# Kernel tuning notes

Hardware: AMD Instinct MI355X
Metric: run time of the kernel (lower is better)

Reference implementation:

```python
import jax, jax.numpy as jnp
import numpy as np

N = 4096
IN_F = 128
OUT_F = 128
H = 4
D = OUT_F // H  # head_out = 32
SLOPE = 0.2
LN_EPS = 1e-5


def setup_inputs() -> dict:
    key = jax.random.key(0)
    k_x, k_adj, k_W, k_a = jax.random.split(key, 4)
    x = jax.random.normal(k_x, (N, IN_F), dtype=jnp.float32)
    adjacency = jax.random.randint(k_adj, (N, N), 0, 2).astype(jnp.bool_)
    # xavier-uniform-ish init scales
    w_std = float(np.sqrt(2.0 / (IN_F + H * D)))
    a_std = float(np.sqrt(2.0 / (H + 2 * D)))
    W = jax.random.normal(k_W, (H * D, IN_F), dtype=jnp.float32) * w_std  # torch Linear weight layout
    a = jax.random.normal(k_a, (H, 2 * D), dtype=jnp.float32) * a_std
    ln_gamma = jnp.ones((OUT_F,), dtype=jnp.float32)
    ln_beta = jnp.zeros((OUT_F,), dtype=jnp.float32)
    return {"x": x, "adjacency": adjacency, "W": W, "a": a,
            "ln_gamma": ln_gamma, "ln_beta": ln_beta}


def reference(x, adjacency, W, a, ln_gamma, ln_beta):
    # Wx: (N, H, D)
    Wx = (x @ W.T).reshape(N, H, D)
    # e[i,j,h] = leaky_relu( <Wx[i,h], a[h,:D]> + <Wx[j,h], a[h,D:]> )
    # (exact factorization of the original cat([Wx_i, Wx_j]) * a sum)
    alpha_i = jnp.einsum('nhd,hd->nh', Wx, a[:, :D])  # source/i term
    alpha_j = jnp.einsum('nhd,hd->nh', Wx, a[:, D:])  # neighbor/j term
    e = alpha_i[:, None, :] + alpha_j[None, :, :]      # (N, N, H)
    e = jnp.where(e >= 0, e, SLOPE * e)                # LeakyReLU
    e = jnp.where(adjacency[:, :, None], e, -jnp.inf)  # mask non-edges
    attn = jax.nn.softmax(e, axis=1)                   # softmax over j
    out = jnp.einsum('ijh,jhd->ihd', attn, Wx).reshape(N, H * D)
    y = out + x                                        # residual (dims match)
    mu = jnp.mean(y, axis=-1, keepdims=True)
    var = jnp.mean((y - mu) ** 2, axis=-1, keepdims=True)
    return ln_gamma * (y - mu) / jnp.sqrt(var + LN_EPS) + ln_beta
```

## Files before the change

kernel.cpp:

```cpp
#include <hip/hip_runtime.h>
#include <hip/hip_bf16.h>
#include <stdint.h>

#define NN 4096
#define SLOPE 0.2f
#define LOG2E 1.44269504088896340736f

typedef float f32x4 __attribute__((ext_vector_type(4)));
typedef float f32x2 __attribute__((ext_vector_type(2)));
typedef short s16x8 __attribute__((ext_vector_type(8)));
typedef unsigned u32x4 __attribute__((ext_vector_type(4)));

static __device__ __forceinline__ unsigned f32_to_bf16_rne(float f) {
    unsigned u = __builtin_bit_cast(unsigned, f);
    return (u + 0x7FFFu + ((u >> 16) & 1u)) >> 16;
}

__global__ __launch_bounds__(256) void k0_pack(const unsigned* __restrict__ src,
                                               unsigned* __restrict__ bits) {
    __shared__ int s_i32;
    const int t = threadIdx.x;
    if (t == 0) {
        int all_small = 1;
        for (int i = 0; i < 32; ++i) all_small &= (src[i] <= 1u);
        s_i32 = all_small;
    }
    __syncthreads();
    const long o = (long)blockIdx.x * 256 + t;
    unsigned m = 0;
    if (s_i32) {
        const u32x4* p = (const u32x4*)src + o * 8;
        #pragma unroll
        for (int g = 0; g < 8; ++g) {
            u32x4 v = p[g];
            m |= (v.x & 1u) << (g * 4) | (v.y & 1u) << (g * 4 + 1) |
                 (v.z & 1u) << (g * 4 + 2) | (v.w & 1u) << (g * 4 + 3);
        }
    } else {
        const u32x4* p = (const u32x4*)src + o * 2;
        #pragma unroll
        for (int g = 0; g < 2; ++g) {
            u32x4 v = p[g];
            unsigned d[4] = {v.x, v.y, v.z, v.w};
            #pragma unroll
            for (int q = 0; q < 4; ++q)
                #pragma unroll
                for (int b = 0; b < 4; ++b)
                    m |= ((d[q] >> (8 * b)) & 1u) << (g * 16 + q * 4 + b);
        }
    }
    bits[o] = m;
}

__global__ __launch_bounds__(256) void k1_wx(const float* __restrict__ x,
                                             const float* __restrict__ W,
                                             const float* __restrict__ a,
                                             unsigned short* __restrict__ wxb,
                                             float* __restrict__ ai_s,
                                             float* __restrict__ ajT_s) {
    __shared__ unsigned short WL[128 * 136];
    __shared__ unsigned short XL[16 * 136];
    __shared__ float WxF[16 * 132];

    const int t = threadIdx.x;
    const int i0 = blockIdx.x * 16;

    for (int p4 = t; p4 < 4096; p4 += 256) {
        f32x4 w4 = *(const f32x4*)(W + 4 * p4);
        unsigned lo = f32_to_bf16_rne(w4.x) | (f32_to_bf16_rne(w4.y) << 16);
        unsigned hi = f32_to_bf16_rne(w4.z) | (f32_to_bf16_rne(w4.w) << 16);
        int c = (4 * p4) >> 7, k = (4 * p4) & 127;
        *(unsigned long long*)&WL[c * 136 + k] =
            (unsigned long long)lo | ((unsigned long long)hi << 32);
    }
    for (int p4 = t; p4 < 512; p4 += 256) {
        f32x4 x4 = *(const f32x4*)(x + (long)i0 * 128 + 4 * p4);
        unsigned lo = f32_to_bf16_rne(x4.x) | (f32_to_bf16_rne(x4.y) << 16);
        unsigned hi = f32_to_bf16_rne(x4.z) | (f32_to_bf16_rne(x4.w) << 16);
        int r = (4 * p4) >> 7, k = (4 * p4) & 127;
        *(unsigned long long*)&XL[r * 136 + k] =
            (unsigned long long)lo | ((unsigned long long)hi << 32);
    }
    __syncthreads();

    const int w = t >> 6, l = t & 63, m = l & 15, q = l >> 4;
    f32x4 acc0 = {0.f, 0.f, 0.f, 0.f}, acc1 = {0.f, 0.f, 0.f, 0.f};
    #pragma unroll
    for (int ks = 0; ks < 4; ++ks) {
        s16x8 af = *(const s16x8*)&XL[m * 136 + ks * 32 + q * 8];
        s16x8 b0 = *(const s16x8*)&WL[(w * 32 + m) * 136 + ks * 32 + q * 8];
        s16x8 b1 = *(const s16x8*)&WL[(w * 32 + 16 + m) * 136 + ks * 32 + q * 8];
        acc0 = __builtin_amdgcn_mfma_f32_16x16x32_bf16(af, b0, acc0, 0, 0, 0);
        acc1 = __builtin_amdgcn_mfma_f32_16x16x32_bf16(af, b1, acc1, 0, 0, 0);
    }
    #pragma unroll
    for (int j2 = 0; j2 < 2; ++j2) {
        const int fblk = 2 * w + j2;
        f32x4 acc = j2 ? acc1 : acc0;
        #pragma unroll
        for (int reg = 0; reg < 4; ++reg) {
            float v = acc[reg];
            int row_g = i0 + q * 4 + reg;
            int kl = row_g & 31, jblk = row_g >> 5;
            wxb[(((jblk * 8 + fblk) * 64 + (kl >> 3) * 16 + m) << 3) + (kl & 7)] =
                (unsigned short)f32_to_bf16_rne(v);
            WxF[(q * 4 + reg) * 132 + fblk * 16 + m] = v;
        }
    }
    __syncthreads();
    if (t < 64) {
        int r = t >> 2, h = t & 3;
        float s_i = 0.f, s_j = 0.f;
        const float* ar = a + h * 64;
        #pragma unroll
        for (int d = 0; d < 32; ++d) {
            float wv = WxF[r * 132 + h * 32 + d];
            s_i += wv * ar[d];
            s_j += wv * ar[32 + d];
        }
        ai_s[(i0 + r) * 4 + h] = s_i * LOG2E;
        ajT_s[h * NN + i0 + r] = s_j * LOG2E;
    }
}

__global__ __launch_bounds__(1024, 4) void k2_attn(
        const float* __restrict__ x,
        const unsigned* __restrict__ adjbits,
        const unsigned short* __restrict__ wxb,
        const float* __restrict__ ai_s,
        const float* __restrict__ ajT_s,
        const float* __restrict__ gamma,
        const float* __restrict__ beta,
        float* __restrict__ out) {
    __shared__ float ajL[4][4096];
    __shared__ unsigned maskL[16][132];
    __shared__ float C_lds[4][16][32];
    __shared__ float l_lds[4][16];

    const int t = threadIdx.x;
    const int i0 = blockIdx.x * 16;
    const int w = t >> 6, l = t & 63;
    const int h = w & 3, p = w >> 2;
    const int m = l & 15, q = l >> 4;

    {
        const f32x4* src = (const f32x4*)ajT_s;
        f32x4* dst = (f32x4*)&ajL[0][0];
        #pragma unroll
        for (int g = 0; g < 4; ++g) dst[t + 1024 * g] = src[t + 1024 * g];
    }
    {
        #pragma unroll
        for (int g = 0; g < 2; ++g) {
            int idx = t + 1024 * g;
            int r = idx >> 7, c = idx & 127;
            maskL[r][c] = adjbits[(long)(i0 + r) * 128 + c];
        }
    }
    const float ai = ai_s[(i0 + m) * 4 + h];
    __syncthreads();

    const unsigned short* bp = wxb + ((2 * h) * 64 + l) * 8;
    const float* ajh = &ajL[h][0] + q * 8;

    f32x4 acc0 = {0.f, 0.f, 0.f, 0.f}, acc1 = {0.f, 0.f, 0.f, 0.f};
    float lpart = 0.f;

    for (int ks = p; ks < 128; ks += 4) {
        unsigned mq = (maskL[m][ks] >> (q * 8)) & 0xffu;
        f32x4 aj0 = *(const f32x4*)(ajh + ks * 32);
        f32x4 aj1 = *(const f32x4*)(ajh + ks * 32 + 4);
        s16x8 b0 = *(const s16x8*)(bp + ks * 4096);
        s16x8 b1 = *(const s16x8*)(bp + ks * 4096 + 512);

        float ev[8];
        #pragma unroll
        for (int e = 0; e < 8; ++e) {
            float s = ai + (e < 4 ? aj0[e] : aj1[e - 4]);
            s = fmaxf(s, SLOPE * s);
            float ex = __builtin_amdgcn_exp2f(s);
            ex = ((mq >> e) & 1u) ? ex : 0.0f;
            lpart += ex;
            ev[e] = ex;
        }
        union { s16x8 v; unsigned u[4]; } af;
        #pragma unroll
        for (int pr = 0; pr < 4; ++pr) {
            unsigned e0 = __builtin_bit_cast(unsigned, ev[2 * pr]);
            unsigned e1 = __builtin_bit_cast(unsigned, ev[2 * pr + 1]);
            af.u[pr] = __builtin_amdgcn_perm(e1, e0, 0x07060302);
        }
        acc0 = __builtin_amdgcn_mfma_f32_16x16x32_bf16(af.v, b0, acc0, 0, 0, 0);
        acc1 = __builtin_amdgcn_mfma_f32_16x16x32_bf16(af.v, b1, acc1, 0, 0, 0);
    }

    lpart += __shfl_xor(lpart, 16, 64);
    lpart += __shfl_xor(lpart, 32, 64);

    if (p == 0) {
        #pragma unroll
        for (int reg = 0; reg < 4; ++reg) {
            C_lds[h][q * 4 + reg][m] = acc0[reg];
            C_lds[h][q * 4 + reg][16 + m] = acc1[reg];
        }
        if (l < 16) l_lds[h][l] = lpart;
    }
    __syncthreads();
    if (p == 1) {
        #pragma unroll
        for (int reg = 0; reg < 4; ++reg) {
            C_lds[h][q * 4 + reg][m] += acc0[reg];
            C_lds[h][q * 4 + reg][16 + m] += acc1[reg];
        }
        if (l < 16) l_lds[h][l] += lpart;
    }
    __syncthreads();
    if (p == 2) {
        #pragma unroll
        for (int reg = 0; reg < 4; ++reg) {
            C_lds[h][q * 4 + reg][m] += acc0[reg];
            C_lds[h][q * 4 + reg][16 + m] += acc1[reg];
        }
        if (l < 16) l_lds[h][l] += lpart;
    }
    __syncthreads();
    if (p == 3) {
        #pragma unroll
        for (int reg = 0; reg < 4; ++reg) {
            C_lds[h][q * 4 + reg][m] += acc0[reg];
            C_lds[h][q * 4 + reg][16 + m] += acc1[reg];
        }
        if (l < 16) l_lds[h][l] += lpart;
    }
    __syncthreads();

    if (t < 512) {
        const int r = t >> 5, c32 = t & 31;
        const int f0 = c32 * 4;
        const int hh = f0 >> 5, cl = f0 & 31;
        const float linv = 1.0f / l_lds[hh][r];
        f32x4 xv = *(const f32x4*)(x + (long)(i0 + r) * 128 + f0);
        float y[4], s1 = 0.f, s2 = 0.f;
        #pragma unroll
        for (int kk = 0; kk < 4; ++kk) {
            float yy = C_lds[hh][r][cl + kk] * linv + xv[kk];
            y[kk] = yy; s1 += yy; s2 += yy * yy;
        }
        #pragma unroll
        for (int s = 1; s <= 16; s <<= 1) {
            s1 += __shfl_xor(s1, s, 64);
            s2 += __shfl_xor(s2, s, 64);
        }
        const float mean = s1 * (1.0f / 128.0f);
        const float var = s2 * (1.0f / 128.0f) - mean * mean;
        const float rstd = rsqrtf(var + 1e-5f);
        f32x4 gv = *(const f32x4*)(gamma + f0);
        f32x4 bv = *(const f32x4*)(beta + f0);
        f32x4 ov;
        #pragma unroll
        for (int kk = 0; kk < 4; ++kk)
            ov[kk] = gv[kk] * ((y[kk] - mean) * rstd) + bv[kk];
        *(f32x4*)(out + (long)(i0 + r) * 128 + f0) = ov;
    }
}

extern "C" void kernel_launch(void* const* d_in, const int* in_sizes, int n_in,
                              void* d_out, int out_size, void* d_ws, size_t ws_size,
                              hipStream_t stream) {
    const float* x = (const float*)d_in[0];
    const unsigned* adj_raw = (const unsigned*)d_in[1];
    const float* W = (const float*)d_in[2];
    const float* a = (const float*)d_in[3];
    const float* gamma = (const float*)d_in[4];
    const float* beta = (const float*)d_in[5];

    unsigned short* wxb = (unsigned short*)d_ws;
    float* ai_s = (float*)((char*)d_ws + (1 << 20));
    float* ajT_s = (float*)((char*)d_ws + (1 << 20) + (64 << 10));
    unsigned* adjbits = (unsigned*)((char*)d_ws + (2 << 20));

    k0_pack<<<2048, 256, 0, stream>>>(adj_raw, adjbits);
    k1_wx<<<256, 256, 0, stream>>>(x, W, a, wxb, ai_s, ajT_s);
    k2_attn<<<256, 1024, 0, stream>>>(x, adjbits, wxb, ai_s, ajT_s, gamma, beta,
                                      (float*)d_out);
}
```

Before: 136.4 us.

## Use fp8/bf8 MFMA for attention aggregation and merge pack and projection kernels

Stores the projected features as fp8 and the attention weights as bf8, so the aggregation runs on the 16x16x32 bf8/fp8 MFMA instead of bf16. The softmax denominator now comes from an extra MFMA against a constant all-ones fp8 vector instead of a scalar sum with shuffles. B-operand loads are prefetched one iteration ahead, and the adjacency-pack and projection kernels are merged into a single launch. This halves the feature bytes and launch count, but costs precision (3-bit mantissa on exp weights, 8-bit fp8 features), which risks tolerance failures.

```diff
diff --git a/kernel.cpp b/kernel.cpp
--- a/kernel.cpp
+++ b/kernel.cpp
@@ -7,7 +7,6 @@
 #define LOG2E 1.44269504088896340736f
 
 typedef float f32x4 __attribute__((ext_vector_type(4)));
-typedef float f32x2 __attribute__((ext_vector_type(2)));
 typedef short s16x8 __attribute__((ext_vector_type(8)));
 typedef unsigned u32x4 __attribute__((ext_vector_type(4)));
 
@@ -16,54 +15,56 @@
     return (u + 0x7FFFu + ((u >> 16) & 1u)) >> 16;
 }
 
-__global__ __launch_bounds__(256) void k0_pack(const unsigned* __restrict__ src,
-                                               unsigned* __restrict__ bits) {
-    __shared__ int s_i32;
+__global__ __launch_bounds__(256) void k01(const unsigned* __restrict__ adj_raw,
+                                           const float* __restrict__ x,
+                                           const float* __restrict__ W,
+                                           const float* __restrict__ a,
+                                           unsigned* __restrict__ bits,
+                                           unsigned* __restrict__ wxb8,
+                                           float* __restrict__ ai_s,
+                                           float* __restrict__ ajT_s) {
     const int t = threadIdx.x;
-    if (t == 0) {
-        int all_small = 1;
-        for (int i = 0; i < 32; ++i) all_small &= (src[i] <= 1u);
-        s_i32 = all_small;
-    }
-    __syncthreads();
-    const long o = (long)blockIdx.x * 256 + t;
-    unsigned m = 0;
-    if (s_i32) {
-        const u32x4* p = (const u32x4*)src + o * 8;
-        #pragma unroll
-        for (int g = 0; g < 8; ++g) {
-            u32x4 v = p[g];
-            m |= (v.x & 1u) << (g * 4) | (v.y & 1u) << (g * 4 + 1) |
-                 (v.z & 1u) << (g * 4 + 2) | (v.w & 1u) << (g * 4 + 3);
-        }
-    } else {
-        const u32x4* p = (const u32x4*)src + o * 2;
-        #pragma unroll
-        for (int g = 0; g < 2; ++g) {
-            u32x4 v = p[g];
-            unsigned d[4] = {v.x, v.y, v.z, v.w};
+    if (blockIdx.x < 2048) {
+        __shared__ int s_i32;
+        if (t == 0) {
+            int all_small = 1;
+            for (int i = 0; i < 32; ++i) all_small &= (adj_raw[i] <= 1u);
+            s_i32 = all_small;
+        }
+        __syncthreads();
+        const long o = (long)blockIdx.x * 256 + t;
+        unsigned mm = 0;
+        if (s_i32) {
+            const u32x4* p = (const u32x4*)adj_raw + o * 8;
             #pragma unroll
-            for (int q = 0; q < 4; ++q)
+            for (int g = 0; g < 8; ++g) {
+                u32x4 v = p[g];
+                mm |= (v.x & 1u) << (g * 4) | (v.y & 1u) << (g * 4 + 1) |
+                      (v.z & 1u) << (g * 4 + 2) | (v.w & 1u) << (g * 4 + 3);
+            }
+        } else {
+            const u32x4* p = (const u32x4*)adj_raw + o * 2;
+            #pragma unroll
+            for (int g = 0; g < 2; ++g) {
+                u32x4 v = p[g];
+                unsigned d[4] = {v.x, v.y, v.z, v.w};
                 #pragma unroll
-                for (int b = 0; b < 4; ++b)
-                    m |= ((d[q] >> (8 * b)) & 1u) << (g * 16 + q * 4 + b);
-        }
-    }
-    bits[o] = m;
-}
-
-__global__ __launch_bounds__(256) void k1_wx(const float* __restrict__ x,
-                                             const float* __restrict__ W,
-                                             const float* __restrict__ a,
-                                             unsigned short* __restrict__ wxb,
-                                             float* __restrict__ ai_s,
-                                             float* __restrict__ ajT_s) {
+                for (int qq = 0; qq < 4; ++qq)
+                    #pragma unroll
+                    for (int b = 0; b < 4; ++b)
+                        mm |= ((d[qq] >> (8 * b)) & 1u) << (g * 16 + qq * 4 + b);
+            }
+        }
+        bits[o] = mm;
+        return;
+    }
+
     __shared__ unsigned short WL[128 * 136];
     __shared__ unsigned short XL[16 * 136];
     __shared__ float WxF[16 * 132];
 
-    const int t = threadIdx.x;
-    const int i0 = blockIdx.x * 16;
+    const int bid = blockIdx.x - 2048;
+    const int i0 = bid * 16;
 
     for (int p4 = t; p4 < 4096; p4 += 256) {
         f32x4 w4 = *(const f32x4*)(W + 4 * p4);
@@ -93,19 +94,18 @@
         acc0 = __builtin_amdgcn_mfma_f32_16x16x32_bf16(af, b0, acc0, 0, 0, 0);
         acc1 = __builtin_amdgcn_mfma_f32_16x16x32_bf16(af, b1, acc1, 0, 0, 0);
     }
+    const int jblk = i0 >> 5;
+    const int qp = ((i0 & 16) + q * 4) >> 3;
+    const int ehalf = q & 1;
     #pragma unroll
     for (int j2 = 0; j2 < 2; ++j2) {
-        const int fblk = 2 * w + j2;
         f32x4 acc = j2 ? acc1 : acc0;
-        #pragma unroll
-        for (int reg = 0; reg < 4; ++reg) {
-            float v = acc[reg];
-            int row_g = i0 + q * 4 + reg;
-            int kl = row_g & 31, jblk = row_g >> 5;
-            wxb[(((jblk * 8 + fblk) * 64 + (kl >> 3) * 16 + m) << 3) + (kl & 7)] =
-                (unsigned short)f32_to_bf16_rne(v);
-            WxF[(q * 4 + reg) * 132 + fblk * 16 + m] = v;
-        }
+        unsigned u = (unsigned)__builtin_amdgcn_cvt_pk_fp8_f32(acc[0], acc[1], 0, false);
+        u = (unsigned)__builtin_amdgcn_cvt_pk_fp8_f32(acc[2], acc[3], (int)u, true);
+        wxb8[(((jblk * 4 + w) * 64 + qp * 16 + m) << 2) + j2 * 2 + ehalf] = u;
+        #pragma unroll
+        for (int reg = 0; reg < 4; ++reg)
+            WxF[(q * 4 + reg) * 132 + (2 * w + j2) * 16 + m] = acc[reg];
     }
     __syncthreads();
     if (t < 64) {
@@ -126,7 +126,7 @@
 __global__ __launch_bounds__(1024, 4) void k2_attn(
         const float* __restrict__ x,
         const unsigned* __restrict__ adjbits,
-        const unsigned short* __restrict__ wxb,
+        const unsigned* __restrict__ wxb8,
         const float* __restrict__ ai_s,
         const float* __restrict__ ajT_s,
         const float* __restrict__ gamma,
@@ -160,18 +160,21 @@
     const float ai = ai_s[(i0 + m) * 4 + h];
     __syncthreads();
 
-    const unsigned short* bp = wxb + ((2 * h) * 64 + l) * 8;
+    const unsigned* bp8 = wxb8 + ((h * 64 + l) << 2);
     const float* ajh = &ajL[h][0] + q * 8;
+    const long ONESB = 0x3838383838383838L;
 
     f32x4 acc0 = {0.f, 0.f, 0.f, 0.f}, acc1 = {0.f, 0.f, 0.f, 0.f};
-    float lpart = 0.f;
-
+    f32x4 accl = {0.f, 0.f, 0.f, 0.f};
+
+    u32x4 bv = *(const u32x4*)(bp8 + (p << 10));
     for (int ks = p; ks < 128; ks += 4) {
+        const int ksn = (ks + 4 < 128) ? (ks + 4) : ks;
+        u32x4 bvn = *(const u32x4*)(bp8 + (ksn << 10));
+
         unsigned mq = (maskL[m][ks] >> (q * 8)) & 0xffu;
         f32x4 aj0 = *(const f32x4*)(ajh + ks * 32);
         f32x4 aj1 = *(const f32x4*)(ajh + ks * 32 + 4);
-        s16x8 b0 = *(const s16x8*)(bp + ks * 4096);
-        s16x8 b1 = *(const s16x8*)(bp + ks * 4096 + 512);
 
         float ev[8];
         #pragma unroll
@@ -179,31 +182,29 @@
             float s = ai + (e < 4 ? aj0[e] : aj1[e - 4]);
             s = fmaxf(s, SLOPE * s);
             float ex = __builtin_amdgcn_exp2f(s);
-            ex = ((mq >> e) & 1u) ? ex : 0.0f;
-            lpart += ex;
-            ev[e] = ex;
-        }
-        union { s16x8 v; unsigned u[4]; } af;
-        #pragma unroll
-        for (int pr = 0; pr < 4; ++pr) {
-            unsigned e0 = __builtin_bit_cast(unsigned, ev[2 * pr]);
-            unsigned e1 = __builtin_bit_cast(unsigned, ev[2 * pr + 1]);
-            af.u[pr] = __builtin_amdgcn_perm(e1, e0, 0x07060302);
-        }
-        acc0 = __builtin_amdgcn_mfma_f32_16x16x32_bf16(af.v, b0, acc0, 0, 0, 0);
-        acc1 = __builtin_amdgcn_mfma_f32_16x16x32_bf16(af.v, b1, acc1, 0, 0, 0);
-    }
-
-    lpart += __shfl_xor(lpart, 16, 64);
-    lpart += __shfl_xor(lpart, 32, 64);
+            ev[e] = ((mq >> e) & 1u) ? ex : 0.0f;
+        }
+        unsigned d0 = (unsigned)__builtin_amdgcn_cvt_pk_bf8_f32(ev[0], ev[1], 0, false);
+        d0 = (unsigned)__builtin_amdgcn_cvt_pk_bf8_f32(ev[2], ev[3], (int)d0, true);
+        unsigned d1 = (unsigned)__builtin_amdgcn_cvt_pk_bf8_f32(ev[4], ev[5], 0, false);
+        d1 = (unsigned)__builtin_amdgcn_cvt_pk_bf8_f32(ev[6], ev[7], (int)d1, true);
+        long av = (long)(((unsigned long long)d1 << 32) | d0);
+        long b0 = (long)(((unsigned long long)bv.y << 32) | bv.x);
+        long b1 = (long)(((unsigned long long)bv.w << 32) | bv.z);
+
+        acc0 = __builtin_amdgcn_mfma_f32_16x16x32_bf8_fp8(av, b0, acc0, 0, 0, 0);
+        acc1 = __builtin_amdgcn_mfma_f32_16x16x32_bf8_fp8(av, b1, acc1, 0, 0, 0);
+        accl = __builtin_amdgcn_mfma_f32_16x16x32_bf8_fp8(av, ONESB, accl, 0, 0, 0);
+        bv = bvn;
+    }
 
     if (p == 0) {
         #pragma unroll
         for (int reg = 0; reg < 4; ++reg) {
             C_lds[h][q * 4 + reg][m] = acc0[reg];
             C_lds[h][q * 4 + reg][16 + m] = acc1[reg];
-        }
-        if (l < 16) l_lds[h][l] = lpart;
+            if (m == 0) l_lds[h][q * 4 + reg] = accl[reg];
+        }
     }
     __syncthreads();
     if (p == 1) {
@@ -211,8 +212,8 @@
         for (int reg = 0; reg < 4; ++reg) {
             C_lds[h][q * 4 + reg][m] += acc0[reg];
             C_lds[h][q * 4 + reg][16 + m] += acc1[reg];
-        }
-        if (l < 16) l_lds[h][l] += lpart;
+            if (m == 0) l_lds[h][q * 4 + reg] += accl[reg];
+        }
     }
     __syncthreads();
     if (p == 2) {
@@ -220,8 +221,8 @@
         for (int reg = 0; reg < 4; ++reg) {
             C_lds[h][q * 4 + reg][m] += acc0[reg];
             C_lds[h][q * 4 + reg][16 + m] += acc1[reg];
-        }
-        if (l < 16) l_lds[h][l] += lpart;
+            if (m == 0) l_lds[h][q * 4 + reg] += accl[reg];
+        }
     }
     __syncthreads();
     if (p == 3) {
@@ -229,8 +230,8 @@
         for (int reg = 0; reg < 4; ++reg) {
             C_lds[h][q * 4 + reg][m] += acc0[reg];
             C_lds[h][q * 4 + reg][16 + m] += acc1[reg];
-        }
-        if (l < 16) l_lds[h][l] += lpart;
+            if (m == 0) l_lds[h][q * 4 + reg] += accl[reg];
+        }
     }
     __syncthreads();
 
@@ -255,11 +256,11 @@
         const float var = s2 * (1.0f / 128.0f) - mean * mean;
         const float rstd = rsqrtf(var + 1e-5f);
         f32x4 gv = *(const f32x4*)(gamma + f0);
-        f32x4 bv = *(const f32x4*)(beta + f0);
+        f32x4 bv2 = *(const f32x4*)(beta + f0);
         f32x4 ov;
         #pragma unroll
         for (int kk = 0; kk < 4; ++kk)
-            ov[kk] = gv[kk] * ((y[kk] - mean) * rstd) + bv[kk];
+            ov[kk] = gv[kk] * ((y[kk] - mean) * rstd) + bv2[kk];
         *(f32x4*)(out + (long)(i0 + r) * 128 + f0) = ov;
     }
 }
@@ -274,13 +275,12 @@
     const float* gamma = (const float*)d_in[4];
     const float* beta = (const float*)d_in[5];
 
-    unsigned short* wxb = (unsigned short*)d_ws;
-    float* ai_s = (float*)((char*)d_ws + (1 << 20));
-    float* ajT_s = (float*)((char*)d_ws + (1 << 20) + (64 << 10));
-    unsigned* adjbits = (unsigned*)((char*)d_ws + (2 << 20));
-
-    k0_pack<<<2048, 256, 0, stream>>>(adj_raw, adjbits);
-    k1_wx<<<256, 256, 0, stream>>>(x, W, a, wxb, ai_s, ajT_s);
-    k2_attn<<<256, 1024, 0, stream>>>(x, adjbits, wxb, ai_s, ajT_s, gamma, beta,
+    unsigned* wxb8 = (unsigned*)d_ws;
+    float* ai_s = (float*)((char*)d_ws + (512 << 10));
+    float* ajT_s = (float*)((char*)d_ws + (576 << 10));
+    unsigned* adjbits = (unsigned*)((char*)d_ws + (1 << 20));
+
+    k01<<<2304, 256, 0, stream>>>(adj_raw, x, W, a, adjbits, wxb8, ai_s, ajT_s);
+    k2_attn<<<256, 1024, 0, stream>>>(x, adjbits, wxb8, ai_s, ajT_s, gamma, beta,
                                       (float*)d_out);
 }
```

After: 135.4 us. Within noise of the previous version (-0.7%).
